# Optimization experiments

Measured on AMD Instinct MI355X. Metric: run time of the kernel, lower is better.

The kernel has to match this reference:

```python
import jax, jax.numpy as jnp
import numpy as np

N = 40000    # nodes
E = 500000   # edges
B = 512      # graphs
NEG_SLOPE = 0.2


def setup_inputs() -> dict:
    key = jax.random.key(0)
    ks = jax.random.split(key, 32)
    p = lambda i, shape: jax.random.normal(ks[i], shape, jnp.float32) * 0.1
    return dict(
        x=jax.random.normal(ks[0], (N, 4), jnp.float32),
        edge_index=jax.random.randint(ks[1], (2, E), 0, N),
        edge_attr=jax.random.normal(ks[2], (E, 1), jnp.float32),
        batch=jnp.sort(jax.random.randint(ks[3], (N,), 0, B)),
        w0=p(4, (1, 4)), b0=p(5, (4,)),
        wl1=p(6, (7, 256)), wr1=p(7, (7, 256)), we1=p(8, (1, 256)), att1=p(9, (8, 32)), b1=p(10, (256,)),
        wl2=p(11, (256, 128)), wr2=p(12, (256, 128)), we2=p(13, (1, 128)), att2=p(14, (8, 16)), b2=p(15, (128,)),
        wl3=p(16, (128, 8)), wr3=p(17, (128, 8)), we3=p(18, (1, 8)), att3=p(19, (1, 8)), b3=p(20, (8,)),
        w4=p(21, (8, 1)), b4=p(22, (1,)),
    )


def _gatv2(x, src, dst, ea, wl, wr, we, att, bias, heads, ch):
    # GATv2Conv: score = att . leaky_relu(Wl x_src + Wr x_dst + We e), segment softmax over dst
    n = x.shape[0]
    xl = (x @ wl).reshape(n, heads, ch)      # source transform [n,H,C]
    xr = (x @ wr).reshape(n, heads, ch)      # target transform
    ee = (ea @ we).reshape(-1, heads, ch)    # edge transform   [Ef,H,C]
    s = jax.nn.leaky_relu(xl[src] + xr[dst] + ee, NEG_SLOPE)
    logits = jnp.einsum('ehc,hc->eh', s, att)
    m = jax.lax.stop_gradient(jax.ops.segment_max(logits, dst, num_segments=n))
    ex = jnp.exp(logits - m[dst])
    denom = jax.ops.segment_sum(ex, dst, num_segments=n)
    alpha = ex / denom[dst]                  # softmax over incoming edges of each node
    out = jax.ops.segment_sum(alpha[:, :, None] * xl[src], dst, num_segments=n)
    return out.reshape(n, heads * ch) + bias


def _forward(x, edge_index, edge_attr, batch,
             w0, b0, wl1, wr1, we1, att1, b1, wl2, wr2, we2, att2, b2,
             wl3, wr3, we3, att3, b3, w4, b4):
    src, dst = edge_index[0], edge_index[1]
    n = x.shape[0]
    # add self loops (PyG default, fill_value='mean' = mean of incoming edge_attr)
    deg = jax.ops.segment_sum(jnp.ones((src.shape[0],), jnp.float32), dst, num_segments=n)
    esum = jax.ops.segment_sum(edge_attr, dst, num_segments=n)
    loop_attr = jnp.where(deg[:, None] > 0, esum / jnp.maximum(deg, 1.0)[:, None], 0.0)
    idx = jnp.arange(n)
    src_f = jnp.concatenate([src, idx])
    dst_f = jnp.concatenate([dst, idx])
    ea_f = jnp.concatenate([edge_attr, loop_attr], axis=0)
    # embed atom type, keep xyz -> 7 features
    h = jnp.concatenate([x[:, :1] @ w0 + b0, x[:, 1:]], axis=1)
    h = jnp.tanh(_gatv2(h, src_f, dst_f, ea_f, wl1, wr1, we1, att1, b1, 8, 32))
    # dropout(p=0.6) is identity in eval mode
    h = jnp.tanh(_gatv2(h, src_f, dst_f, ea_f, wl2, wr2, we2, att2, b2, 8, 16))
    h = jnp.tanh(_gatv2(h, src_f, dst_f, ea_f, wl3, wr3, we3, att3, b3, 1, 8))
    # scatter-mean pooling per graph
    cnt = jax.ops.segment_sum(jnp.ones((n,), jnp.float32), batch, num_segments=B)
    pooled = jax.ops.segment_sum(h, batch, num_segments=B) / jnp.maximum(cnt, 1.0)[:, None]
    return pooled @ w4 + b4  # [B,1]


def reference(x, edge_index, edge_attr, batch, w0, b0, wl1, wr1, we1, att1, b1,
              wl2, wr2, we2, att2, b2, wl3, wr3, we3, att3, b3, w4, b4):
    return _forward(x, edge_index, edge_attr, batch, w0, b0, wl1, wr1, we1, att1, b1,
                    wl2, wr2, we2, att2, b2, wl3, wr3, we3, att3, b3, w4, b4)
```

## Files before the change

kernel.cpp:

```cpp
#include <hip/hip_runtime.h>
#include <math.h>

#define NN 40000
#define NNP 40192
#define NE 500000
#define NEF (NN + NE)
#define NB 512
#define NEG 0.2f
#define NBLK_C 157

static inline int cdiv(int a, int b) { return (a + b - 1) / b; }

typedef __attribute__((ext_vector_type(8))) short short8;
typedef __attribute__((ext_vector_type(4))) short short4v;
typedef __attribute__((ext_vector_type(4))) float f32x4;
typedef __attribute__((ext_vector_type(2))) _Float16 half2v;

__device__ __forceinline__ unsigned short f2bf(float f) {
  unsigned u = __float_as_uint(f);
  unsigned r = (u + 0x7fffu + ((u >> 16) & 1u)) >> 16;
  return (unsigned short)r;
}
__device__ __forceinline__ float bf2f(unsigned short h) {
  return __uint_as_float((unsigned)h << 16);
}
__device__ __forceinline__ float lrelu(float v) {
  return fmaxf(v, NEG * v);
}
__device__ __forceinline__ float red8(float p) {
  p += __uint_as_float((unsigned)__builtin_amdgcn_mov_dpp((int)__float_as_uint(p), 0xB1, 0xF, 0xF, true));
  p += __uint_as_float((unsigned)__builtin_amdgcn_mov_dpp((int)__float_as_uint(p), 0x4E, 0xF, 0xF, true));
  p += __uint_as_float((unsigned)__builtin_amdgcn_mov_dpp((int)__float_as_uint(p), 0x141, 0xF, 0xF, true));
  return p;
}

__global__ void k_deg(const int* __restrict__ ei, const float* __restrict__ ea,
                      int* __restrict__ degi, float* __restrict__ esum) {
  int e = blockIdx.x * 256 + threadIdx.x;
  if (e < NE) {
    int d = ei[NE + e];
    atomicAdd(degi + d, 1);
    atomicAdd(esum + d, ea[e]);
  }
}

__global__ void k_scanA(const int* __restrict__ degi, int* __restrict__ pre,
                        int* __restrict__ bsum, float* __restrict__ lpa,
                        const int* __restrict__ bat, int* __restrict__ gstart) {
  __shared__ int sh[256];
  int t = threadIdx.x, i = blockIdx.x * 256 + t;
  int dg = i < NN ? degi[i] : -1;
  sh[t] = i < NN ? dg + 1 : 0;
  if (i < NN) {
    lpa[i] = dg > 0 ? lpa[i] / (float)dg : 0.f;
    int b = bat[i];
    int bp = i > 0 ? bat[i - 1] : -1;
    for (int g = bp + 1; g <= b; g++) gstart[g] = i;
    if (i == NN - 1)
      for (int g = b + 1; g <= NB; g++) gstart[g] = NN;
  }
  __syncthreads();
  for (int st = 1; st < 256; st <<= 1) {
    int a = t >= st ? sh[t - st] : 0;
    __syncthreads();
    sh[t] += a;
    __syncthreads();
  }
  if (i < NN) pre[i] = sh[t];
  if (t == 255) bsum[blockIdx.x] = sh[255];
}

__global__ void k_scan3(const int* __restrict__ pre, const int* __restrict__ bsum,
                        int* __restrict__ rowptr) {
  __shared__ int sh[256];
  int t = threadIdx.x;
  sh[t] = t < NBLK_C ? bsum[t] : 0;
  __syncthreads();
  for (int st = 1; st < 256; st <<= 1) {
    int a = t >= st ? sh[t - st] : 0;
    __syncthreads();
    sh[t] += a;
    __syncthreads();
  }
  int i = blockIdx.x * 256 + t;
  if (i < NN) {
    int off = blockIdx.x > 0 ? sh[blockIdx.x - 1] : 0;
    rowptr[i + 1] = pre[i] + off;
    if (i == 0) rowptr[0] = 0;
  }
}

__global__ void k_fill(const int* __restrict__ ei, const float* __restrict__ ea,
                       const float* __restrict__ lpa, const int* __restrict__ rowptr,
                       int* __restrict__ fillc, int2* __restrict__ cedge) {
  int e = blockIdx.x * 256 + threadIdx.x;
  if (e >= NEF) return;
  int s, d;
  float v;
  if (e < NE) { s = ei[e]; d = ei[NE + e]; v = ea[e]; }
  else        { s = e - NE; d = s; v = lpa[s]; }
  int pos = atomicAdd(fillc + d, 1);
  int idx = rowptr[d] + pos;
  cedge[idx] = make_int2(s, __float_as_int(v));
}

__global__ __launch_bounds__(256) void k_gat1(const int* __restrict__ rowptr,
                                              const int2* __restrict__ cedge,
                                              const float* __restrict__ xx,
                                              const float* __restrict__ w0,
                                              const float* __restrict__ b0,
                                              const float* __restrict__ wl,
                                              const float* __restrict__ wr,
                                              const float* __restrict__ we,
                                              const float* __restrict__ att,
                                              const float* __restrict__ bias,
                                              short* __restrict__ ah,
                                              short* __restrict__ al) {
  const int lane = threadIdx.x & 63;
  const int node = __builtin_amdgcn_readfirstlane(blockIdx.x * 4 + (threadIdx.x >> 6));
  const int j0 = lane * 4;
  if (node >= NN) {
    short4v z = {0, 0, 0, 0};
    *(short4v*)(ah + (size_t)node * 256 + j0) = z;
    *(short4v*)(al + (size_t)node * 256 + j0) = z;
    return;
  }

  float4 wev = *(const float4*)(we + j0);
  float4 attv = *(const float4*)(att + j0);
  float w0s[4] = {w0[0], w0[1], w0[2], w0[3]};
  float b0s[4] = {b0[0], b0[1], b0[2], b0[3]};
  float u[4] = {0.f, 0.f, 0.f, 0.f}, v[4] = {0.f, 0.f, 0.f, 0.f};
#pragma unroll
  for (int j = 0; j < 4; j++) {
    float4 t = *(const float4*)(wl + j * 256 + j0);
    float tt[4] = {t.x, t.y, t.z, t.w};
#pragma unroll
    for (int c = 0; c < 4; c++) {
      u[c] = fmaf(w0s[j], tt[c], u[c]);
      v[c] = fmaf(b0s[j], tt[c], v[c]);
    }
  }
  float4 wl4 = *(const float4*)(wl + 4 * 256 + j0);
  float4 wl5 = *(const float4*)(wl + 5 * 256 + j0);
  float4 wl6 = *(const float4*)(wl + 6 * 256 + j0);

  float xrr[4] = {0.f, 0.f, 0.f, 0.f};
  {
    float4 xv = *(const float4*)(xx + (size_t)node * 4);
    float hn[7] = {fmaf(xv.x, w0s[0], b0s[0]), fmaf(xv.x, w0s[1], b0s[1]),
                   fmaf(xv.x, w0s[2], b0s[2]), fmaf(xv.x, w0s[3], b0s[3]),
                   xv.y, xv.z, xv.w};
#pragma unroll
    for (int k = 0; k < 7; k++) {
      float4 t = *(const float4*)(wr + k * 256 + j0);
      xrr[0] = fmaf(hn[k], t.x, xrr[0]);
      xrr[1] = fmaf(hn[k], t.y, xrr[1]);
      xrr[2] = fmaf(hn[k], t.z, xrr[2]);
      xrr[3] = fmaf(hn[k], t.w, xrr[3]);
    }
  }

  float m = -INFINITY, den = 0.f;
  float acc[4] = {0.f, 0.f, 0.f, 0.f};
  const int kb = rowptr[node], ke = rowptr[node + 1];

#define G1_EDGE(XS, EAV)                                                        \
  {                                                                             \
    float xls[4];                                                               \
    _Pragma("unroll")                                                           \
    for (int c = 0; c < 4; c++) xls[c] = fmaf((XS).x, u[c], v[c]);              \
    xls[0] = fmaf((XS).y, wl4.x, xls[0]); xls[1] = fmaf((XS).y, wl4.y, xls[1]); \
    xls[2] = fmaf((XS).y, wl4.z, xls[2]); xls[3] = fmaf((XS).y, wl4.w, xls[3]); \
    xls[0] = fmaf((XS).z, wl5.x, xls[0]); xls[1] = fmaf((XS).z, wl5.y, xls[1]); \
    xls[2] = fmaf((XS).z, wl5.z, xls[2]); xls[3] = fmaf((XS).z, wl5.w, xls[3]); \
    xls[0] = fmaf((XS).w, wl6.x, xls[0]); xls[1] = fmaf((XS).w, wl6.y, xls[1]); \
    xls[2] = fmaf((XS).w, wl6.z, xls[2]); xls[3] = fmaf((XS).w, wl6.w, xls[3]); \
    float p = 0.f;                                                              \
    p = fmaf(lrelu(xls[0] + fmaf((EAV), wev.x, xrr[0])), attv.x, p);            \
    p = fmaf(lrelu(xls[1] + fmaf((EAV), wev.y, xrr[1])), attv.y, p);            \
    p = fmaf(lrelu(xls[2] + fmaf((EAV), wev.z, xrr[2])), attv.z, p);            \
    p = fmaf(lrelu(xls[3] + fmaf((EAV), wev.w, xrr[3])), attv.w, p);            \
    p = red8(p);                                                                \
    if (!__all(p <= m + 8.f)) {                                                 \
      float mn = fmaxf(m, p);                                                   \
      float sc = __expf(m - mn);                                                \
      den *= sc;                                                                \
      _Pragma("unroll")                                                         \
      for (int c = 0; c < 4; c++) acc[c] *= sc;                                 \
      m = mn;                                                                   \
    }                                                                           \
    float ex = __expf(p - m);                                                   \
    den += ex;                                                                  \
    _Pragma("unroll")                                                           \
    for (int c = 0; c < 4; c++) acc[c] = fmaf(ex, xls[c], acc[c]);              \
  }

  int i1 = kb + 1 < ke ? kb + 1 : ke - 1;
  int2 edA = cedge[kb], edB = cedge[i1];
  float4 xA = *(const float4*)(xx + (size_t)edA.x * 4);
  float4 xB = *(const float4*)(xx + (size_t)edB.x * 4);
  for (int k = kb; k < ke; k += 2) {
    const int i2 = k + 2 < ke ? k + 2 : ke - 1;
    const int i3 = k + 3 < ke ? k + 3 : ke - 1;
    const int2 edC = cedge[i2], edD = cedge[i3];
    const float4 xC = *(const float4*)(xx + (size_t)edC.x * 4);
    const float4 xD = *(const float4*)(xx + (size_t)edD.x * 4);
    G1_EDGE(xA, __int_as_float(edA.y));
    if (k + 1 < ke) {
      G1_EDGE(xB, __int_as_float(edB.y));
    }
    xA = xC; edA = edC; xB = xD; edB = edD;
  }
#undef G1_EDGE

  float rd = 1.f / den;
  float4 bv = *(const float4*)(bias + j0);
  float bb[4] = {bv.x, bv.y, bv.z, bv.w};
  short hi[4], lo[4];
#pragma unroll
  for (int c = 0; c < 4; c++) {
    float hv = tanhf(fmaf(acc[c], rd, bb[c]));
    unsigned short hb = f2bf(hv);
    hi[c] = (short)hb;
    lo[c] = (short)f2bf(hv - bf2f(hb));
  }
  *(short4v*)(ah + (size_t)node * 256 + j0) = *(short4v*)hi;
  *(short4v*)(al + (size_t)node * 256 + j0) = *(short4v*)lo;
}

__global__ void k_wsplit(const float* __restrict__ wl, const float* __restrict__ wr,
                         short* __restrict__ bh, short* __restrict__ bl) {
  int id = blockIdx.x * 256 + threadIdx.x;
  int n = id >> 8, k = id & 255;
  float w = n < 128 ? wl[k * 128 + n] : wr[k * 128 + n - 128];
  unsigned short hb = f2bf(w);
  bh[n * 256 + k] = (short)hb;
  bl[n * 256 + k] = (short)f2bf(w - bf2f(hb));
}

__global__ __launch_bounds__(256) void k_gemm2(const short* __restrict__ ah,
                                               const short* __restrict__ al,
                                               const short* __restrict__ bh,
                                               const short* __restrict__ bl,
                                               _Float16* __restrict__ xlh,
                                               float* __restrict__ xr) {
  __shared__ short sAh[128 * 40];
  __shared__ short sAl[128 * 40];
  __shared__ short sBh[64 * 40];
  __shared__ short sBl[64 * 40];
  const int tid = threadIdx.x;
  const int bm = blockIdx.x >> 2, bn = blockIdx.x & 3;
  const int wid = tid >> 6, lane = tid & 63;
  const int wr = wid >> 1, wc = wid & 1;
  const int l15 = lane & 15, lhi = lane >> 4;
  const int srow = tid >> 2;
  const int kq = (tid & 3) * 8;
  f32x4 acc[4][2];
#pragma unroll
  for (int a = 0; a < 4; a++)
#pragma unroll
    for (int b = 0; b < 2; b++) acc[a][b] = (f32x4)(0.f);

#pragma unroll 1
  for (int st = 0; st < 8; st++) {
    const int k0 = st * 32;
    const long aoff0 = (long)(bm * 128 + srow) * 256 + k0 + kq;
    const long aoff1 = aoff0 + 64 * 256;
    const long boff = (long)(bn * 64 + srow) * 256 + k0 + kq;
    short8 vah0 = *(const short8*)(ah + aoff0);
    short8 vah1 = *(const short8*)(ah + aoff1);
    short8 val0 = *(const short8*)(al + aoff0);
    short8 val1 = *(const short8*)(al + aoff1);
    short8 vbh  = *(const short8*)(bh + boff);
    short8 vbl  = *(const short8*)(bl + boff);
    __syncthreads();
    *(short8*)&sAh[srow * 40 + kq] = vah0;
    *(short8*)&sAh[(64 + srow) * 40 + kq] = vah1;
    *(short8*)&sAl[srow * 40 + kq] = val0;
    *(short8*)&sAl[(64 + srow) * 40 + kq] = val1;
    *(short8*)&sBh[srow * 40 + kq] = vbh;
    *(short8*)&sBl[srow * 40 + kq] = vbl;
    __syncthreads();
    short8 bfh[2], bfl[2];
#pragma unroll
    for (int fn = 0; fn < 2; fn++) {
      bfh[fn] = *(const short8*)&sBh[(wc * 32 + fn * 16 + l15) * 40 + lhi * 8];
      bfl[fn] = *(const short8*)&sBl[(wc * 32 + fn * 16 + l15) * 40 + lhi * 8];
    }
#pragma unroll
    for (int fm = 0; fm < 4; fm++) {
      short8 afh = *(const short8*)&sAh[(wr * 64 + fm * 16 + l15) * 40 + lhi * 8];
      short8 afl = *(const short8*)&sAl[(wr * 64 + fm * 16 + l15) * 40 + lhi * 8];
      acc[fm][0] = __builtin_amdgcn_mfma_f32_16x16x32_bf16(afh, bfh[0], acc[fm][0], 0, 0, 0);
      acc[fm][1] = __builtin_amdgcn_mfma_f32_16x16x32_bf16(afh, bfh[1], acc[fm][1], 0, 0, 0);
      acc[fm][0] = __builtin_amdgcn_mfma_f32_16x16x32_bf16(afh, bfl[0], acc[fm][0], 0, 0, 0);
      acc[fm][1] = __builtin_amdgcn_mfma_f32_16x16x32_bf16(afh, bfl[1], acc[fm][1], 0, 0, 0);
      acc[fm][0] = __builtin_amdgcn_mfma_f32_16x16x32_bf16(afl, bfh[0], acc[fm][0], 0, 0, 0);
      acc[fm][1] = __builtin_amdgcn_mfma_f32_16x16x32_bf16(afl, bfh[1], acc[fm][1], 0, 0, 0);
    }
  }
#pragma unroll
  for (int fm = 0; fm < 4; fm++)
#pragma unroll
    for (int fn = 0; fn < 2; fn++) {
      int col = bn * 64 + wc * 32 + fn * 16 + l15;
#pragma unroll
      for (int j = 0; j < 4; j++) {
        int row = bm * 128 + wr * 64 + fm * 16 + lhi * 4 + j;
        if (col < 128) xlh[(long)row * 128 + col] = (_Float16)acc[fm][fn][j];
        else           xr[(long)row * 128 + col - 128] = acc[fm][fn][j];
      }
    }
}

__global__ __launch_bounds__(256) void k_gat2(const int* __restrict__ rowptr,
                                              const int2* __restrict__ cedge,
                                              const _Float16* __restrict__ xlh,
                                              const float* __restrict__ xr,
                                              const float* __restrict__ we,
                                              const float* __restrict__ att,
                                              const float* __restrict__ bias,
                                              float* __restrict__ hout) {
  const int lane = threadIdx.x & 63;
  const int node = __builtin_amdgcn_readfirstlane(blockIdx.x * 4 + (threadIdx.x >> 6));
  if (node >= NN) return;
  const int j0 = lane * 2;
  float2 xrr = *(const float2*)(xr + (long)node * 128 + j0);
  float2 wev = *(const float2*)(we + j0);
  float2 attv = *(const float2*)(att + j0);
  float m = -INFINITY, den = 0.f, acc0 = 0.f, acc1 = 0.f;
  const int kb = rowptr[node], ke = rowptr[node + 1];

#define G2_EDGE(AV, EAV)                                                  \
  {                                                                       \
    float av0 = (float)(AV).x, av1 = (float)(AV).y;                       \
    float v0 = lrelu(av0 + fmaf((EAV), wev.x, xrr.x));                    \
    float v1 = lrelu(av1 + fmaf((EAV), wev.y, xrr.y));                    \
    float p = red8(fmaf(v0, attv.x, v1 * attv.y));                        \
    if (!__all(p <= m + 8.f)) {                                           \
      float mn = fmaxf(m, p);                                             \
      float sc = __expf(m - mn);                                          \
      den *= sc;                                                          \
      acc0 *= sc;                                                         \
      acc1 *= sc;                                                         \
      m = mn;                                                             \
    }                                                                     \
    float ex = __expf(p - m);                                             \
    den += ex;                                                            \
    acc0 = fmaf(ex, av0, acc0);                                           \
    acc1 = fmaf(ex, av1, acc1);                                           \
  }

  int i1 = kb + 1 < ke ? kb + 1 : ke - 1;
  int2 edA = cedge[kb], edB = cedge[i1];
  half2v aA = *(const half2v*)(xlh + (long)edA.x * 128 + j0);
  half2v aB = *(const half2v*)(xlh + (long)edB.x * 128 + j0);
  for (int k = kb; k < ke; k += 2) {
    const int i2 = k + 2 < ke ? k + 2 : ke - 1;
    const int i3 = k + 3 < ke ? k + 3 : ke - 1;
    const int2 edC = cedge[i2], edD = cedge[i3];
    const half2v aC = *(const half2v*)(xlh + (long)edC.x * 128 + j0);
    const half2v aD = *(const half2v*)(xlh + (long)edD.x * 128 + j0);
    G2_EDGE(aA, __int_as_float(edA.y));
    if (k + 1 < ke) {
      G2_EDGE(aB, __int_as_float(edB.y));
    }
    aA = aC; edA = edC; aB = aD; edB = edD;
  }
#undef G2_EDGE

  float rd = 1.f / den;
  hout[(long)node * 128 + j0]     = tanhf(fmaf(acc0, rd, bias[j0]));
  hout[(long)node * 128 + j0 + 1] = tanhf(fmaf(acc1, rd, bias[j0 + 1]));
}

__global__ __launch_bounds__(256) void k_mm3(const float* __restrict__ h,
                                             const float* __restrict__ wl,
                                             const float* __restrict__ wr,
                                             float* __restrict__ xl,
                                             float* __restrict__ xr) {
  __shared__ float srow[64 * 132];
  __shared__ float lw[128 * 16];
  const int t = threadIdx.x;
  const int n0 = blockIdx.x * 64;
#pragma unroll
  for (int q = 0; q < 8; q++) {
    int gi = (t + q * 256) * 4;
    int row = gi >> 7, col = gi & 127;
    float4 v = *(const float4*)(h + (size_t)(n0 + row) * 128 + col);
    *(float4*)&srow[row * 132 + col] = v;
  }
#pragma unroll
  for (int q = 0; q < 8; q++) {
    int idx = t + q * 256;
    int k = idx >> 4, j = idx & 15;
    lw[idx] = j < 8 ? wl[k * 8 + j] : wr[k * 8 + (j - 8)];
  }
  __syncthreads();
  const int nid = t >> 2, g = t & 3;
  float a0 = 0.f, a1 = 0.f, a2 = 0.f, a3 = 0.f;
  const float* rp = &srow[nid * 132];
  for (int k = 0; k < 128; k++) {
    float hv = rp[k];
    float4 w = *(const float4*)&lw[k * 16 + g * 4];
    a0 = fmaf(hv, w.x, a0);
    a1 = fmaf(hv, w.y, a1);
    a2 = fmaf(hv, w.z, a2);
    a3 = fmaf(hv, w.w, a3);
  }
  float4 r = {a0, a1, a2, a3};
  int node = n0 + nid;
  float* dst = (g & 2) ? xr : xl;
  *(float4*)(dst + node * 8 + (g & 1) * 4) = r;
}

__global__ __launch_bounds__(256) void k_gat3(const int* __restrict__ rowptr,
                                              const int2* __restrict__ cedge,
                                              const float* __restrict__ xl,
                                              const float* __restrict__ xr,
                                              const float* __restrict__ we,
                                              const float* __restrict__ att,
                                              const float* __restrict__ bias,
                                              float* __restrict__ hout) {
  const int lane = threadIdx.x & 7;
  const int node = blockIdx.x * 32 + (threadIdx.x >> 3);
  if (node >= NN) return;
  const float xrr = xr[node * 8 + lane];
  const float wev = we[lane];
  const float attv = att[lane];
  float m = -INFINITY, den = 0.f, acc = 0.f;
  const int kb = rowptr[node], ke = rowptr[node + 1];

#define G3_EDGE(AV, EAV)                                      \
  {                                                           \
    float v = lrelu((AV) + fmaf((EAV), wev, xrr));            \
    float p = red8(v * attv);                                 \
    if (p > m + 8.f) {                                        \
      float mn = fmaxf(m, p);                                 \
      float sc = __expf(m - mn);                              \
      den *= sc;                                              \
      acc *= sc;                                              \
      m = mn;                                                 \
    }                                                         \
    float ex = __expf(p - m);                                 \
    den += ex;                                                \
    acc = fmaf(ex, (AV), acc);                                \
  }

  int i1 = kb + 1 < ke ? kb + 1 : ke - 1;
  int2 edA = cedge[kb], edB = cedge[i1];
  float aA = xl[edA.x * 8 + lane];
  float aB = xl[edB.x * 8 + lane];
  for (int k = kb; k < ke; k += 2) {
    const int i2 = k + 2 < ke ? k + 2 : ke - 1;
    const int i3 = k + 3 < ke ? k + 3 : ke - 1;
    const int2 edC = cedge[i2], edD = cedge[i3];
    const float aC = xl[edC.x * 8 + lane];
    const float aD = xl[edD.x * 8 + lane];
    G3_EDGE(aA, __int_as_float(edA.y));
    if (k + 1 < ke) {
      G3_EDGE(aB, __int_as_float(edB.y));
    }
    aA = aC; edA = edC; aB = aD; edB = edD;
  }
#undef G3_EDGE

  hout[node * 8 + lane] = tanhf(acc / den + bias[lane]);
}

__global__ __launch_bounds__(256) void k_poolG(const int* __restrict__ gstart,
                                               const float* __restrict__ h3,
                                               const float* __restrict__ w4,
                                               const float* __restrict__ b4,
                                               float* __restrict__ out) {
  const int lane = threadIdx.x & 63;
  const int g = blockIdx.x * 4 + (threadIdx.x >> 6);
  if (g >= NB) return;
  const int kb = gstart[g], ke = gstart[g + 1];
  const int ch = lane & 7, no = lane >> 3;
  float acc = 0.f;
  for (int n = kb + no; n < ke; n += 8)
    acc += h3[(size_t)n * 8 + ch];
  acc += __shfl_xor(acc, 8);
  acc += __shfl_xor(acc, 16);
  acc += __shfl_xor(acc, 32);
  float cnt = fmaxf((float)(ke - kb), 1.f);
  float yv = (acc / cnt) * w4[ch];
  yv = red8(yv);
  if (lane == 0) out[g] = yv + b4[0];
}

extern "C" void kernel_launch(void* const* d_in, const int* in_sizes, int n_in,
                              void* d_out, int out_size, void* d_ws, size_t ws_size,
                              hipStream_t stream) {
  const float* x   = (const float*)d_in[0];
  const int*   ei  = (const int*)d_in[1];
  const float* ea  = (const float*)d_in[2];
  const int*   bat = (const int*)d_in[3];
  const float* w0  = (const float*)d_in[4];
  const float* b0  = (const float*)d_in[5];
  const float* wl1 = (const float*)d_in[6];
  const float* wr1 = (const float*)d_in[7];
  const float* we1 = (const float*)d_in[8];
  const float* at1 = (const float*)d_in[9];
  const float* b1  = (const float*)d_in[10];
  const float* wl2 = (const float*)d_in[11];
  const float* wr2 = (const float*)d_in[12];
  const float* we2 = (const float*)d_in[13];
  const float* at2 = (const float*)d_in[14];
  const float* b2  = (const float*)d_in[15];
  const float* wl3 = (const float*)d_in[16];
  const float* wr3 = (const float*)d_in[17];
  const float* we3 = (const float*)d_in[18];
  const float* at3 = (const float*)d_in[19];
  const float* b3  = (const float*)d_in[20];
  const float* w4  = (const float*)d_in[21];
  const float* b4  = (const float*)d_in[22];
  float* out = (float*)d_out;

  char* W = (char*)d_ws;
  size_t o = 0;
  auto alloc = [&](size_t bytes) { void* p = W + o; o += (bytes + 255) & ~(size_t)255; return p; };
  int*      degi   = (int*)alloc(NN * 4);
  int*      fillc  = (int*)alloc(NN * 4);
  float*    lpa    = (float*)alloc(NN * 4);
  int*      rowptr = (int*)alloc((NN + 1) * 4);
  int*      pre    = (int*)alloc(NN * 4);
  int*      bsum   = (int*)alloc(256 * 4);
  int*      gstart = (int*)alloc((NB + 1) * 4);
  int2*     cedge  = (int2*)alloc((size_t)NEF * 8);
  short*    Ah     = (short*)alloc((size_t)NNP * 256 * 2);
  short*    Al     = (short*)alloc((size_t)NNP * 256 * 2);
  short*    Bh     = (short*)alloc((size_t)256 * 256 * 2);
  short*    Bl     = (short*)alloc((size_t)256 * 256 * 2);
  _Float16* Xlh2   = (_Float16*)alloc((size_t)NNP * 128 * 2);
  float*    Xr2    = (float*)alloc((size_t)NNP * 128 * 4);
  float*    H2     = (float*)alloc((size_t)NN * 128 * 4);
  float*    Xl3    = (float*)alloc((size_t)NN * 8 * 4);
  float*    Xr3    = (float*)alloc((size_t)NN * 8 * 4);
  float*    H3     = (float*)alloc((size_t)NN * 8 * 4);
  (void)ws_size; (void)in_sizes; (void)n_in; (void)out_size;

  const int NBLK = cdiv(NN, 256);

  hipMemsetAsync(degi, 0, 3 * NN * 4, stream);
  k_deg<<<cdiv(NE, 256), 256, 0, stream>>>(ei, ea, degi, lpa);
  k_scanA<<<NBLK, 256, 0, stream>>>(degi, pre, bsum, lpa, bat, gstart);
  k_scan3<<<NBLK, 256, 0, stream>>>(pre, bsum, rowptr);
  k_fill<<<cdiv(NEF, 256), 256, 0, stream>>>(ei, ea, lpa, rowptr, fillc, cedge);

  k_gat1<<<NNP / 4, 256, 0, stream>>>(rowptr, cedge, x, w0, b0, wl1, wr1, we1, at1, b1, Ah, Al);

  k_wsplit<<<256, 256, 0, stream>>>(wl2, wr2, Bh, Bl);
  k_gemm2<<<(NNP / 128) * 4, 256, 0, stream>>>(Ah, Al, Bh, Bl, Xlh2, Xr2);
  k_gat2<<<cdiv(NN, 4), 256, 0, stream>>>(rowptr, cedge, Xlh2, Xr2, we2, at2, b2, H2);

  k_mm3<<<NN / 64, 256, 0, stream>>>(H2, wl3, wr3, Xl3, Xr3);
  k_gat3<<<cdiv(NN, 32), 256, 0, stream>>>(rowptr, cedge, Xl3, Xr3, we3, at3, b3, H3);

  k_poolG<<<cdiv(NB, 4), 256, 0, stream>>>(gstart, H3, w4, b4, out);
}
```

Before: 234.6 us.

## Fuse layer-3 linear transform into GAT2 epilogue and swizzle GEMM2 blocks

Folds the layer-3 projection (128→8 for source and target) into the end of the layer-2 attention kernel. Each wave stages its node's tanh output in shared memory and does a small dot product against a transposed weight matrix, which k_wsplit now also prepares. This removes the H2 round trip through global memory and one kernel launch. The GEMM2 block index is also remapped across eight groups to change the order in which tiles are scheduled, at the cost of some extra per-node work in gat2.

```diff
diff --git a/kernel.cpp b/kernel.cpp
--- a/kernel.cpp
+++ b/kernel.cpp
@@ -230,13 +230,21 @@
 }
 
 __global__ void k_wsplit(const float* __restrict__ wl, const float* __restrict__ wr,
-                         short* __restrict__ bh, short* __restrict__ bl) {
+                         short* __restrict__ bh, short* __restrict__ bl,
+                         const float* __restrict__ wl3, const float* __restrict__ wr3,
+                         float* __restrict__ w3t) {
   int id = blockIdx.x * 256 + threadIdx.x;
-  int n = id >> 8, k = id & 255;
-  float w = n < 128 ? wl[k * 128 + n] : wr[k * 128 + n - 128];
-  unsigned short hb = f2bf(w);
-  bh[n * 256 + k] = (short)hb;
-  bl[n * 256 + k] = (short)f2bf(w - bf2f(hb));
+  if (id < 65536) {
+    int n = id >> 8, k = id & 255;
+    float w = n < 128 ? wl[k * 128 + n] : wr[k * 128 + n - 128];
+    unsigned short hb = f2bf(w);
+    bh[n * 256 + k] = (short)hb;
+    bl[n * 256 + k] = (short)f2bf(w - bf2f(hb));
+  } else if (id < 65536 + 2048) {
+    int t = id - 65536;
+    int j = t >> 7, k = t & 127;
+    w3t[j * 128 + k] = j < 8 ? wl3[k * 8 + j] : wr3[k * 8 + (j - 8)];
+  }
 }
 
 __global__ __launch_bounds__(256) void k_gemm2(const short* __restrict__ ah,
@@ -250,7 +258,8 @@
   __shared__ short sBh[64 * 40];
   __shared__ short sBl[64 * 40];
   const int tid = threadIdx.x;
-  const int bm = blockIdx.x >> 2, bn = blockIdx.x & 3;
+  const int wgid = (blockIdx.x & 7) * ((NNP / 128) * 4 / 8) + (blockIdx.x >> 3);
+  const int bm = wgid >> 2, bn = wgid & 3;
   const int wid = tid >> 6, lane = tid & 63;
   const int wr = wid >> 1, wc = wid & 1;
   const int l15 = lane & 15, lhi = lane >> 4;
@@ -321,9 +330,13 @@
                                               const float* __restrict__ we,
                                               const float* __restrict__ att,
                                               const float* __restrict__ bias,
-                                              float* __restrict__ hout) {
+                                              const float* __restrict__ w3t,
+                                              float* __restrict__ xl3,
+                                              float* __restrict__ xr3) {
+  __shared__ float h2s[4][128];
   const int lane = threadIdx.x & 63;
-  const int node = __builtin_amdgcn_readfirstlane(blockIdx.x * 4 + (threadIdx.x >> 6));
+  const int w = threadIdx.x >> 6;
+  const int node = __builtin_amdgcn_readfirstlane(blockIdx.x * 4 + w);
   if (node >= NN) return;
   const int j0 = lane * 2;
   float2 xrr = *(const float2*)(xr + (long)node * 128 + j0);
@@ -371,48 +384,30 @@
 #undef G2_EDGE
 
   float rd = 1.f / den;
-  hout[(long)node * 128 + j0]     = tanhf(fmaf(acc0, rd, bias[j0]));
-  hout[(long)node * 128 + j0 + 1] = tanhf(fmaf(acc1, rd, bias[j0 + 1]));
-}
-
-__global__ __launch_bounds__(256) void k_mm3(const float* __restrict__ h,
-                                             const float* __restrict__ wl,
-                                             const float* __restrict__ wr,
-                                             float* __restrict__ xl,
-                                             float* __restrict__ xr) {
-  __shared__ float srow[64 * 132];
-  __shared__ float lw[128 * 16];
-  const int t = threadIdx.x;
-  const int n0 = blockIdx.x * 64;
-#pragma unroll
-  for (int q = 0; q < 8; q++) {
-    int gi = (t + q * 256) * 4;
-    int row = gi >> 7, col = gi & 127;
-    float4 v = *(const float4*)(h + (size_t)(n0 + row) * 128 + col);
-    *(float4*)&srow[row * 132 + col] = v;
-  }
-#pragma unroll
-  for (int q = 0; q < 8; q++) {
-    int idx = t + q * 256;
-    int k = idx >> 4, j = idx & 15;
-    lw[idx] = j < 8 ? wl[k * 8 + j] : wr[k * 8 + (j - 8)];
-  }
-  __syncthreads();
-  const int nid = t >> 2, g = t & 3;
-  float a0 = 0.f, a1 = 0.f, a2 = 0.f, a3 = 0.f;
-  const float* rp = &srow[nid * 132];
-  for (int k = 0; k < 128; k++) {
-    float hv = rp[k];
-    float4 w = *(const float4*)&lw[k * 16 + g * 4];
-    a0 = fmaf(hv, w.x, a0);
-    a1 = fmaf(hv, w.y, a1);
-    a2 = fmaf(hv, w.z, a2);
-    a3 = fmaf(hv, w.w, a3);
-  }
-  float4 r = {a0, a1, a2, a3};
-  int node = n0 + nid;
-  float* dst = (g & 2) ? xr : xl;
-  *(float4*)(dst + node * 8 + (g & 1) * 4) = r;
+  float t0 = tanhf(fmaf(acc0, rd, bias[j0]));
+  float t1 = tanhf(fmaf(acc1, rd, bias[j0 + 1]));
+  float2 tw = {t0, t1};
+  *(float2*)&h2s[w][j0] = tw;
+
+  const int j = lane & 15, q = lane >> 4;
+  const float* hp = &h2s[w][q * 32];
+  const float* wp = w3t + j * 128 + q * 32;
+  float a3 = 0.f;
+#pragma unroll
+  for (int i = 0; i < 8; i++) {
+    float4 hv = *(const float4*)(hp + i * 4);
+    float4 wv = *(const float4*)(wp + i * 4);
+    a3 = fmaf(hv.x, wv.x, a3);
+    a3 = fmaf(hv.y, wv.y, a3);
+    a3 = fmaf(hv.z, wv.z, a3);
+    a3 = fmaf(hv.w, wv.w, a3);
+  }
+  a3 += __shfl_xor(a3, 16);
+  a3 += __shfl_xor(a3, 32);
+  if (lane < 16) {
+    if (j < 8) xl3[node * 8 + j] = a3;
+    else       xr3[node * 8 + (j - 8)] = a3;
+  }
 }
 
 __global__ __launch_bounds__(256) void k_gat3(const int* __restrict__ rowptr,
@@ -534,9 +529,9 @@
   short*    Al     = (short*)alloc((size_t)NNP * 256 * 2);
   short*    Bh     = (short*)alloc((size_t)256 * 256 * 2);
   short*    Bl     = (short*)alloc((size_t)256 * 256 * 2);
+  float*    W3t    = (float*)alloc(16 * 128 * 4);
   _Float16* Xlh2   = (_Float16*)alloc((size_t)NNP * 128 * 2);
   float*    Xr2    = (float*)alloc((size_t)NNP * 128 * 4);
-  float*    H2     = (float*)alloc((size_t)NN * 128 * 4);
   float*    Xl3    = (float*)alloc((size_t)NN * 8 * 4);
   float*    Xr3    = (float*)alloc((size_t)NN * 8 * 4);
   float*    H3     = (float*)alloc((size_t)NN * 8 * 4);
@@ -552,11 +547,10 @@
 
   k_gat1<<<NNP / 4, 256, 0, stream>>>(rowptr, cedge, x, w0, b0, wl1, wr1, we1, at1, b1, Ah, Al);
 
-  k_wsplit<<<256, 256, 0, stream>>>(wl2, wr2, Bh, Bl);
+  k_wsplit<<<264, 256, 0, stream>>>(wl2, wr2, Bh, Bl, wl3, wr3, W3t);
   k_gemm2<<<(NNP / 128) * 4, 256, 0, stream>>>(Ah, Al, Bh, Bl, Xlh2, Xr2);
-  k_gat2<<<cdiv(NN, 4), 256, 0, stream>>>(rowptr, cedge, Xlh2, Xr2, we2, at2, b2, H2);
-
-  k_mm3<<<NN / 64, 256, 0, stream>>>(H2, wl3, wr3, Xl3, Xr3);
+  k_gat2<<<cdiv(NN, 4), 256, 0, stream>>>(rowptr, cedge, Xlh2, Xr2, we2, at2, b2, W3t, Xl3, Xr3);
+
   k_gat3<<<cdiv(NN, 32), 256, 0, stream>>>(rowptr, cedge, Xl3, Xr3, we3, at3, b3, H3);
 
   k_poolG<<<cdiv(NB, 4), 256, 0, stream>>>(gstart, H3, w4, b4, out);
```

Result: no change. 237.4 us (+1.2%).
